# Kernel tuning notes

Measured on AMD Instinct MI355X. Metric: run time of the kernel, lower is better.

The kernel has to match this reference:

```python
import jax, jax.numpy as jnp
import numpy as np

B, S, HID = 1, 4096, 2048
H, KV, D = 16, 4, 128          # query heads, kv heads, head_dim
REP = H // KV                   # GQA group size
SCALE = 0.08838834764831845     # query_pre_attn_scalar (= head_dim**-0.5)
SOFTCAP = 50.0                  # attn_logit_softcapping
NEG = -1e9


def rotate_half(x):
    x1, x2 = jnp.split(x, 2, axis=-1)
    return jnp.concatenate((-x2, x1), axis=-1)


def setup_inputs() -> dict:
    key = jax.random.key(0)
    ks = jax.random.split(key, 8)
    hidden_states = jax.random.normal(ks[0], (B, S, HID), jnp.float32)
    # RoPE tables [B, S, D]
    inv_freq = 1.0 / (10000.0 ** (np.arange(0, D, 2, dtype=np.float32) / D))
    pos = np.arange(S, dtype=np.float32)
    freqs = np.outer(pos, inv_freq)                      # [S, D/2]
    emb = np.concatenate([freqs, freqs], axis=-1)        # [S, D]
    cos = jnp.asarray(np.cos(emb))[None]                 # [1, S, D]
    sin = jnp.asarray(np.sin(emb))[None]
    # additive causal mask [1, 1, S, S]
    causal = jnp.tril(jnp.ones((S, S), jnp.bool_))
    attention_mask = jnp.where(causal, 0.0, NEG)[None, None].astype(jnp.float32)
    wq = jax.random.normal(ks[1], (H * D, HID), jnp.float32) * 0.02
    wk = jax.random.normal(ks[2], (KV * D, HID), jnp.float32) * 0.02
    wv = jax.random.normal(ks[3], (KV * D, HID), jnp.float32) * 0.02
    wo = jax.random.normal(ks[4], (HID, H * D), jnp.float32) * 0.02
    return {"hidden_states": hidden_states, "cos": cos, "sin": sin,
            "attention_mask": attention_mask, "wq": wq, "wk": wk, "wv": wv, "wo": wo}


def reference(hidden_states, cos, sin, attention_mask, wq, wk, wv, wo):
    b, s, _ = hidden_states.shape
    # projections (nn.Linear: x @ W^T)
    q = (hidden_states @ wq.T).reshape(b, s, H, D).transpose(0, 2, 1, 3)   # [b,H,s,D]
    k = (hidden_states @ wk.T).reshape(b, s, KV, D).transpose(0, 2, 1, 3)  # [b,KV,s,D]
    v = (hidden_states @ wv.T).reshape(b, s, KV, D).transpose(0, 2, 1, 3)
    # RoPE (cos/sin broadcast over head dim)
    c = cos[:, None]  # [b,1,s,D]
    sn = sin[:, None]
    q = q * c + rotate_half(q) * sn
    k = k * c + rotate_half(k) * sn
    q = q * SCALE
    # GQA: group query heads instead of materializing repeated K/V
    qg = q.reshape(b, KV, REP, s, D)                                       # [b,g,r,s,D]
    scores = jnp.einsum('bgrqd,bgkd->bgrqk', qg, k)                        # [b,g,r,s,s]
    scores = jnp.tanh(scores / SOFTCAP) * SOFTCAP
    scores = scores + attention_mask[:, :, None]                           # broadcast mask
    probs = jax.nn.softmax(scores.astype(jnp.float32), axis=-1).astype(q.dtype)
    out = jnp.einsum('bgrqk,bgkd->bgrqd', probs, v)                        # [b,g,r,s,D]
    out = out.reshape(b, H, s, D).transpose(0, 2, 1, 3).reshape(b, s, H * D)
    return out @ wo.T
```

## Files before the change

kernel.cpp:

```cpp
#include <hip/hip_runtime.h>
#include <stdint.h>


typedef __attribute__((ext_vector_type(8))) short bf16x8;
typedef __attribute__((ext_vector_type(4))) float f32x4;

#define SCALE_F 0.08838834764831845f

__device__ __forceinline__ ushort f2bf(float f) {
  union { float f; uint32_t u; } v; v.f = f;
  uint32_t r = (v.u + 0x7FFFu + ((v.u >> 16) & 1u)) >> 16;
  return (ushort)r;
}
__device__ __forceinline__ ushort f2bf_fast(float f) {
  union { float f; uint32_t u; } v; v.f = f;
  return (ushort)((v.u + 0x8000u) >> 16);
}
__device__ __forceinline__ float bf2f(ushort u) {
  union { uint32_t u; float f; } v; v.u = ((uint32_t)u) << 16;
  return v.f;
}
__device__ __forceinline__ void gload_lds16(const void* g, void* l) {
  __builtin_amdgcn_global_load_lds((__attribute__((address_space(1))) void*)g,
                                   (__attribute__((address_space(3))) void*)l,
                                   16, 0, 0);
}

__global__ void cvt_kernel(const float* __restrict__ src, ushort* __restrict__ dst, int n4) {
  int idx = blockIdx.x * blockDim.x + threadIdx.x;
  int stride = gridDim.x * blockDim.x;
  for (int i = idx; i < n4; i += stride) {
    float4 v = ((const float4*)src)[i];
    ushort4 o;
    o.x = f2bf(v.x); o.y = f2bf(v.y); o.z = f2bf(v.z); o.w = f2bf(v.w);
    ((ushort4*)dst)[i] = o;
  }
}

template <int MODE>
__global__ __launch_bounds__(256, 2) void gemm_bt(
    const ushort* __restrict__ A, const ushort* __restrict__ B,
    ushort* __restrict__ Cbf, float* __restrict__ Cf, ushort* __restrict__ Vt,
    int M, int N, int K, int ldc) {
  __shared__ ushort As[128 * 64];
  __shared__ ushort Bs[128 * 64];
  const int tid = threadIdx.x;
  const int m0 = blockIdx.y * 128;
  const int n0 = blockIdx.x * 128;
  const int lane = tid & 63, w = tid >> 6;
  const int wr = (w >> 1) * 64, wc = (w & 1) * 64;
  const int fr = lane & 15, fg = lane >> 4;

  const f32x4 vzero = {0.f, 0.f, 0.f, 0.f};
  f32x4 acc[4][4];
#pragma unroll
  for (int i = 0; i < 4; ++i)
#pragma unroll
    for (int j = 0; j < 4; ++j) acc[i][j] = vzero;

  for (int kt = 0; kt < K; kt += 64) {
    __syncthreads();
#pragma unroll
    for (int jj = 0; jj < 4; ++jj) {
      int ci = jj * 256 + tid;
      int r = ci >> 3, c = ci & 7;
      int cs = c ^ (r & 7);
      gload_lds16(A + ((size_t)(m0 + r) * K + kt + cs * 8), &As[ci * 8]);
      gload_lds16(B + ((size_t)(n0 + r) * K + kt + cs * 8), &Bs[ci * 8]);
    }
    __syncthreads();
#pragma unroll
    for (int kk = 0; kk < 2; ++kk) {
      bf16x8 aF[4], bF[4];
#pragma unroll
      for (int i = 0; i < 4; ++i) {
        int r = wr + i * 16 + fr;
        int c = kk * 4 + fg;
        aF[i] = *(const bf16x8*)&As[r * 64 + ((c ^ (r & 7)) * 8)];
      }
#pragma unroll
      for (int j = 0; j < 4; ++j) {
        int r = wc + j * 16 + fr;
        int c = kk * 4 + fg;
        bF[j] = *(const bf16x8*)&Bs[r * 64 + ((c ^ (r & 7)) * 8)];
      }
#pragma unroll
      for (int i = 0; i < 4; ++i)
#pragma unroll
        for (int j = 0; j < 4; ++j)
          acc[i][j] = __builtin_amdgcn_mfma_f32_16x16x32_bf16(aF[i], bF[j], acc[i][j], 0, 0, 0);
    }
  }

  if (MODE == 0) {
    if (n0 < 2560) {
#pragma unroll
      for (int i = 0; i < 4; ++i)
#pragma unroll
        for (int j = 0; j < 4; ++j) {
          int m = m0 + wr + i * 16 + fg * 4;
          int n = n0 + wc + j * 16 + fr;
#pragma unroll
          for (int r = 0; r < 4; ++r)
            Cbf[(size_t)(m + r) * ldc + n] = f2bf(acc[i][j][r]);
        }
    } else {
#pragma unroll
      for (int i = 0; i < 4; ++i)
#pragma unroll
        for (int j = 0; j < 4; ++j) {
          int d = (n0 - 2560) + wc + j * 16 + fr;
          int mB = m0 + wr + i * 16 + fg * 4;
          ushort4 pv;
          pv.x = f2bf(acc[i][j][0]);
          pv.y = f2bf(acc[i][j][1]);
          pv.z = f2bf(acc[i][j][2]);
          pv.w = f2bf(acc[i][j][3]);
          *(ushort4*)&Vt[(size_t)d * 4096 + mB] = pv;
        }
    }
  } else {
#pragma unroll
    for (int i = 0; i < 4; ++i)
#pragma unroll
      for (int j = 0; j < 4; ++j) {
        int m = m0 + wr + i * 16 + fg * 4;
        int n = n0 + wc + j * 16 + fr;
#pragma unroll
        for (int r = 0; r < 4; ++r)
          Cf[(size_t)(m + r) * ldc + n] = acc[i][j][r];
      }
  }
}

__global__ void rope_kernel(ushort* __restrict__ QKV, const float* __restrict__ cosp,
                            const float* __restrict__ sinp) {
  int id = blockIdx.x * blockDim.x + threadIdx.x;
  int s = id / 160;
  int rem = id % 160;
  int head = rem >> 3;
  int d0 = (rem & 7) * 8;
  size_t base = (size_t)s * 2560 + head * 128 + d0;
  bf16x8 lo = *(bf16x8*)&QKV[base];
  bf16x8 hi = *(bf16x8*)&QKV[base + 64];
  const float* cr = cosp + (size_t)s * 128 + d0;
  const float* sr = sinp + (size_t)s * 128 + d0;
  float scale = (head < 16) ? SCALE_F : 1.0f;
  bf16x8 vlo, vhi;
#pragma unroll
  for (int e = 0; e < 8; ++e) {
    float lv = bf2f((ushort)lo[e]);
    float hv = bf2f((ushort)hi[e]);
    float c = cr[e], sn = sr[e];
    float nlo = (lv * c - hv * sn) * scale;
    float nhi = (hv * c + lv * sn) * scale;
    vlo[e] = (short)f2bf(nlo);
    vhi[e] = (short)f2bf(nhi);
  }
  *(bf16x8*)&QKV[base] = vlo;
  *(bf16x8*)&QKV[base + 64] = vhi;
}

__global__ __launch_bounds__(256, 2) void attn_kernel(
    const ushort* __restrict__ QKV, const ushort* __restrict__ Vt,
    ushort* __restrict__ Out) {
  __shared__ ushort Ks[2][64 * 128];
  __shared__ ushort Vs[2][128 * 64];
  __shared__ ushort Ps[4][32 * 64];

  const int tid = threadIdx.x;
  const int x = blockIdx.x;
  const int qb = (x < 256) ? (x >> 4) : (47 - (x >> 4));
  const int h = x & 15;
  const int g = h >> 2;
  const int lane = tid & 63, w = tid >> 6;
  const int fr = lane & 15, fg = lane >> 4;
  const int q0 = qb * 128 + w * 32;

  bf16x8 qf[2][4];
#pragma unroll
  for (int i = 0; i < 2; ++i)
#pragma unroll
    for (int kk = 0; kk < 4; ++kk)
      qf[i][kk] = *(const bf16x8*)&QKV[(size_t)(q0 + i * 16 + fr) * 2560 + h * 128 + kk * 32 + fg * 8];

  const f32x4 vzero = {0.f, 0.f, 0.f, 0.f};
  float lrow[2][4];
  f32x4 Oa[2][8];
#pragma unroll
  for (int i = 0; i < 2; ++i) {
#pragma unroll
    for (int r = 0; r < 4; ++r) lrow[i][r] = 0.f;
#pragma unroll
    for (int jd = 0; jd < 8; ++jd) Oa[i][jd] = vzero;
  }

  const int nt = 2 * qb + 2;
  const size_t kcol = 2048 + (size_t)g * 128;
  const size_t vbase = (size_t)g * 128 * 4096;
  ushort* pw = &Ps[w][0];

  const float K1 = 0.05770780163555854f;
  const float K2 = -144.26950408889634f;

  auto stage = [&](int buf, int t) {
#pragma unroll
    for (int jj = 0; jj < 4; ++jj) {
      int ci = jj * 256 + tid;
      {
        int r = ci >> 4, c = ci & 15;
        int cs = c ^ (r & 7);
        gload_lds16(&QKV[(size_t)(t * 64 + r) * 2560 + kcol + cs * 8], &Ks[buf][ci * 8]);
      }
      {
        int r = ci >> 3, c = ci & 7;
        int cs = c ^ (r & 7);
        gload_lds16(&Vt[vbase + (size_t)r * 4096 + t * 64 + cs * 8], &Vs[buf][ci * 8]);
      }
    }
  };

  stage(0, 0);
  __syncthreads();

  for (int t = 0; t < nt; ++t) {
    const int cur = t & 1;
    if (t + 1 < nt) stage(cur ^ 1, t + 1);

    const bool skipw = (t == nt - 1) && (w < 2);
    if (!skipw) {
      f32x4 sv[2][4];
#pragma unroll
      for (int i = 0; i < 2; ++i)
#pragma unroll
        for (int j = 0; j < 4; ++j) sv[i][j] = vzero;
      __builtin_amdgcn_s_setprio(1);
#pragma unroll
      for (int kk = 0; kk < 4; ++kk) {
#pragma unroll
        for (int j = 0; j < 4; ++j) {
          int r = j * 16 + fr;
          int c = kk * 4 + fg;
          bf16x8 bF = *(const bf16x8*)&Ks[cur][r * 128 + ((c ^ (r & 7)) * 8)];
#pragma unroll
          for (int i = 0; i < 2; ++i)
            sv[i][j] = __builtin_amdgcn_mfma_f32_16x16x32_bf16(qf[i][kk], bF, sv[i][j], 0, 0, 0);
        }
      }
      __builtin_amdgcn_s_setprio(0);

      const bool need_mask = ((t == nt - 2) && (w < 2)) || ((t == nt - 1) && (w >= 2));

#pragma unroll
      for (int i = 0; i < 2; ++i)
#pragma unroll
        for (int j = 0; j < 4; ++j)
#pragma unroll
          for (int r = 0; r < 4; ++r) {
            float v = sv[i][j][r];
            float ex = exp2f(v * K1);
            float p = exp2f(K2 * __builtin_amdgcn_rcpf(ex + 1.0f));
            if (need_mask) {
              int row = q0 + i * 16 + fg * 4 + r;
              int col = t * 64 + j * 16 + fr;
              p = (col > row) ? 0.f : p;
            }
            lrow[i][r] += p;
            sv[i][j][r] = p;
          }

#pragma unroll
      for (int i = 0; i < 2; ++i)
#pragma unroll
        for (int j = 0; j < 4; ++j)
#pragma unroll
          for (int r = 0; r < 4; ++r) {
            int rr = i * 16 + fg * 4 + r;
            int cc = j * 16 + fr;
            int addr = rr * 64 + (((cc >> 3) ^ (rr & 7)) * 8) + (cc & 7);
            pw[addr] = f2bf_fast(sv[i][j][r]);
          }

      __builtin_amdgcn_s_setprio(1);
#pragma unroll
      for (int kk = 0; kk < 2; ++kk) {
        bf16x8 paf[2];
#pragma unroll
        for (int i = 0; i < 2; ++i) {
          int r = i * 16 + fr;
          int c = kk * 4 + fg;
          paf[i] = *(const bf16x8*)&pw[r * 64 + ((c ^ (r & 7)) * 8)];
        }
#pragma unroll
        for (int jd = 0; jd < 8; ++jd) {
          int rv = jd * 16 + fr;
          int c = kk * 4 + fg;
          bf16x8 vF = *(const bf16x8*)&Vs[cur][rv * 64 + ((c ^ (rv & 7)) * 8)];
#pragma unroll
          for (int i = 0; i < 2; ++i)
            Oa[i][jd] = __builtin_amdgcn_mfma_f32_16x16x32_bf16(paf[i], vF, Oa[i][jd], 0, 0, 0);
        }
      }
      __builtin_amdgcn_s_setprio(0);
    }

    __syncthreads();
  }

#pragma unroll
  for (int i = 0; i < 2; ++i)
#pragma unroll
    for (int r = 0; r < 4; ++r) {
      float s = lrow[i][r];
      s += __shfl_xor(s, 1, 64);
      s += __shfl_xor(s, 2, 64);
      s += __shfl_xor(s, 4, 64);
      s += __shfl_xor(s, 8, 64);
      float inv = __builtin_amdgcn_rcpf(s);
      int m = q0 + i * 16 + fg * 4 + r;
#pragma unroll
      for (int jd = 0; jd < 8; ++jd)
        Out[(size_t)m * 2048 + h * 128 + jd * 16 + fr] = f2bf(Oa[i][jd][r] * inv);
    }
}

extern "C" void kernel_launch(void* const* d_in, const int* in_sizes, int n_in,
                              void* d_out, int out_size, void* d_ws, size_t ws_size,
                              hipStream_t stream) {
  const float* hidden = (const float*)d_in[0];
  const float* cosp = (const float*)d_in[1];
  const float* sinp = (const float*)d_in[2];
  const float* wq = (const float*)d_in[4];
  const float* wk = (const float*)d_in[5];
  const float* wv = (const float*)d_in[6];
  const float* wo = (const float*)d_in[7];
  float* out = (float*)d_out;

  char* ws = (char*)d_ws;
  ushort* Xb = (ushort*)(ws);
  ushort* Wqkv = (ushort*)(ws + 16777216);
  ushort* Wob = (ushort*)(ws + 16777216 + 12582912);
  ushort* QKV = (ushort*)(ws + 16777216 + 12582912 + 8388608);
  ushort* Vtb = (ushort*)(ws + 16777216 + 12582912 + 8388608 + 20971520);
  ushort* AttnO = Xb;

  cvt_kernel<<<2048, 256, 0, stream>>>(hidden, Xb, (4096 * 2048) / 4);
  cvt_kernel<<<1024, 256, 0, stream>>>(wq, Wqkv, (2048 * 2048) / 4);
  cvt_kernel<<<512, 256, 0, stream>>>(wk, Wqkv + 2048 * 2048, (512 * 2048) / 4);
  cvt_kernel<<<512, 256, 0, stream>>>(wv, Wqkv + 2560 * 2048, (512 * 2048) / 4);
  cvt_kernel<<<1024, 256, 0, stream>>>(wo, Wob, (2048 * 2048) / 4);

  gemm_bt<0><<<dim3(24, 32), 256, 0, stream>>>(Xb, Wqkv, QKV, nullptr, Vtb,
                                               4096, 3072, 2048, 2560);
  rope_kernel<<<2560, 256, 0, stream>>>(QKV, cosp, sinp);
  attn_kernel<<<512, 256, 0, stream>>>(QKV, Vtb, AttnO);
  gemm_bt<1><<<dim3(16, 32), 256, 0, stream>>>(AttnO, Wob, nullptr, out, nullptr,
                                               4096, 2048, 2048, 2048);
}
```

Measured before the change: 437.3 us.

## Split causal attention KV range across two blocks and add normalization pass

Each (query block, head) pair now launches as two blocks, each covering half of the causal key tiles. Each half writes unnormalized fp32 partial outputs and row sums to workspace, and a new norm_kernel adds the halves, divides by the row sums and converts to bf16. Because the softcapped softmax uses a fixed maximum, the partial sums can be added directly without rescaling. The aim is more blocks and better load balance across CUs, at the cost of extra fp32 memory traffic and an additional kernel launch. The split path runs only when the workspace is large enough to hold the partial buffers.

```diff
diff --git a/kernel.cpp b/kernel.cpp
--- a/kernel.cpp
+++ b/kernel.cpp
@@ -161,17 +161,26 @@
   *(bf16x8*)&QKV[base + 64] = vhi;
 }
 
+template <int SPLIT>
 __global__ __launch_bounds__(256, 2) void attn_kernel(
     const ushort* __restrict__ QKV, const ushort* __restrict__ Vt,
-    ushort* __restrict__ Out) {
+    ushort* __restrict__ Out, float* __restrict__ pO, float* __restrict__ pl) {
   __shared__ ushort Ks[2][64 * 128];
   __shared__ ushort Vs[2][128 * 64];
   __shared__ ushort Ps[4][32 * 64];
 
   const int tid = threadIdx.x;
   const int x = blockIdx.x;
-  const int qb = (x < 256) ? (x >> 4) : (47 - (x >> 4));
-  const int h = x & 15;
+  int qb, h, c;
+  if (SPLIT) {
+    qb = 31 - (x >> 5);
+    h = x & 15;
+    c = (x >> 4) & 1;
+  } else {
+    qb = (x < 256) ? (x >> 4) : (47 - (x >> 4));
+    h = x & 15;
+    c = 0;
+  }
   const int g = h >> 2;
   const int lane = tid & 63, w = tid >> 6;
   const int fr = lane & 15, fg = lane >> 4;
@@ -196,6 +205,8 @@
   }
 
   const int nt = 2 * qb + 2;
+  const int t0 = SPLIT ? c * (qb + 1) : 0;
+  const int t1 = SPLIT ? (t0 + qb + 1) : nt;
   const size_t kcol = 2048 + (size_t)g * 128;
   const size_t vbase = (size_t)g * 128 * 4096;
   ushort* pw = &Ps[w][0];
@@ -208,24 +219,24 @@
     for (int jj = 0; jj < 4; ++jj) {
       int ci = jj * 256 + tid;
       {
-        int r = ci >> 4, c = ci & 15;
-        int cs = c ^ (r & 7);
+        int r = ci >> 4, cc = ci & 15;
+        int cs = cc ^ (r & 7);
         gload_lds16(&QKV[(size_t)(t * 64 + r) * 2560 + kcol + cs * 8], &Ks[buf][ci * 8]);
       }
       {
-        int r = ci >> 3, c = ci & 7;
-        int cs = c ^ (r & 7);
+        int r = ci >> 3, cc = ci & 7;
+        int cs = cc ^ (r & 7);
         gload_lds16(&Vt[vbase + (size_t)r * 4096 + t * 64 + cs * 8], &Vs[buf][ci * 8]);
       }
     }
   };
 
-  stage(0, 0);
+  stage(0, t0);
   __syncthreads();
 
-  for (int t = 0; t < nt; ++t) {
-    const int cur = t & 1;
-    if (t + 1 < nt) stage(cur ^ 1, t + 1);
+  for (int t = t0; t < t1; ++t) {
+    const int cur = (t - t0) & 1;
+    if (t + 1 < t1) stage(cur ^ 1, t + 1);
 
     const bool skipw = (t == nt - 1) && (w < 2);
     if (!skipw) {
@@ -240,8 +251,8 @@
 #pragma unroll
         for (int j = 0; j < 4; ++j) {
           int r = j * 16 + fr;
-          int c = kk * 4 + fg;
-          bf16x8 bF = *(const bf16x8*)&Ks[cur][r * 128 + ((c ^ (r & 7)) * 8)];
+          int cc = kk * 4 + fg;
+          bf16x8 bF = *(const bf16x8*)&Ks[cur][r * 128 + ((cc ^ (r & 7)) * 8)];
 #pragma unroll
           for (int i = 0; i < 2; ++i)
             sv[i][j] = __builtin_amdgcn_mfma_f32_16x16x32_bf16(qf[i][kk], bF, sv[i][j], 0, 0, 0);
@@ -288,14 +299,14 @@
 #pragma unroll
         for (int i = 0; i < 2; ++i) {
           int r = i * 16 + fr;
-          int c = kk * 4 + fg;
-          paf[i] = *(const bf16x8*)&pw[r * 64 + ((c ^ (r & 7)) * 8)];
+          int cc = kk * 4 + fg;
+          paf[i] = *(const bf16x8*)&pw[r * 64 + ((cc ^ (r & 7)) * 8)];
         }
 #pragma unroll
         for (int jd = 0; jd < 8; ++jd) {
           int rv = jd * 16 + fr;
-          int c = kk * 4 + fg;
-          bf16x8 vF = *(const bf16x8*)&Vs[cur][rv * 64 + ((c ^ (rv & 7)) * 8)];
+          int cc = kk * 4 + fg;
+          bf16x8 vF = *(const bf16x8*)&Vs[cur][rv * 64 + ((cc ^ (rv & 7)) * 8)];
 #pragma unroll
           for (int i = 0; i < 2; ++i)
             Oa[i][jd] = __builtin_amdgcn_mfma_f32_16x16x32_bf16(paf[i], vF, Oa[i][jd], 0, 0, 0);
@@ -307,21 +318,58 @@
     __syncthreads();
   }
 
-#pragma unroll
-  for (int i = 0; i < 2; ++i)
-#pragma unroll
-    for (int r = 0; r < 4; ++r) {
-      float s = lrow[i][r];
-      s += __shfl_xor(s, 1, 64);
-      s += __shfl_xor(s, 2, 64);
-      s += __shfl_xor(s, 4, 64);
-      s += __shfl_xor(s, 8, 64);
-      float inv = __builtin_amdgcn_rcpf(s);
-      int m = q0 + i * 16 + fg * 4 + r;
-#pragma unroll
-      for (int jd = 0; jd < 8; ++jd)
-        Out[(size_t)m * 2048 + h * 128 + jd * 16 + fr] = f2bf(Oa[i][jd][r] * inv);
-    }
+  if (SPLIT) {
+    float* pOc = pO + (size_t)c * 4096 * 2048;
+#pragma unroll
+    for (int i = 0; i < 2; ++i)
+#pragma unroll
+      for (int r = 0; r < 4; ++r) {
+        float s = lrow[i][r];
+        s += __shfl_xor(s, 1, 64);
+        s += __shfl_xor(s, 2, 64);
+        s += __shfl_xor(s, 4, 64);
+        s += __shfl_xor(s, 8, 64);
+        int m = q0 + i * 16 + fg * 4 + r;
+        if (fr == 0) pl[(size_t)c * 4096 * 16 + m * 16 + h] = s;
+#pragma unroll
+        for (int jd = 0; jd < 8; ++jd)
+          pOc[(size_t)m * 2048 + h * 128 + jd * 16 + fr] = Oa[i][jd][r];
+      }
+  } else {
+#pragma unroll
+    for (int i = 0; i < 2; ++i)
+#pragma unroll
+      for (int r = 0; r < 4; ++r) {
+        float s = lrow[i][r];
+        s += __shfl_xor(s, 1, 64);
+        s += __shfl_xor(s, 2, 64);
+        s += __shfl_xor(s, 4, 64);
+        s += __shfl_xor(s, 8, 64);
+        float inv = __builtin_amdgcn_rcpf(s);
+        int m = q0 + i * 16 + fg * 4 + r;
+#pragma unroll
+        for (int jd = 0; jd < 8; ++jd)
+          Out[(size_t)m * 2048 + h * 128 + jd * 16 + fr] = f2bf(Oa[i][jd][r] * inv);
+      }
+  }
+}
+
+__global__ void norm_kernel(const float* __restrict__ pO, const float* __restrict__ pl,
+                            ushort* __restrict__ Out) {
+  int i = blockIdx.x * blockDim.x + threadIdx.x;
+  int col = (i * 4) & 2047;
+  int m = (i * 4) >> 11;
+  int h = col >> 7;
+  float l = pl[m * 16 + h] + pl[4096 * 16 + m * 16 + h];
+  float inv = __builtin_amdgcn_rcpf(l);
+  float4 a = ((const float4*)pO)[i];
+  float4 b = ((const float4*)pO)[i + (4096 * 2048 / 4)];
+  ushort4 o;
+  o.x = f2bf((a.x + b.x) * inv);
+  o.y = f2bf((a.y + b.y) * inv);
+  o.z = f2bf((a.z + b.z) * inv);
+  o.w = f2bf((a.w + b.w) * inv);
+  ((ushort4*)Out)[i] = o;
 }
 
 extern "C" void kernel_launch(void* const* d_in, const int* in_sizes, int n_in,
@@ -337,11 +385,15 @@
   float* out = (float*)d_out;
 
   char* ws = (char*)d_ws;
-  ushort* Xb = (ushort*)(ws);
-  ushort* Wqkv = (ushort*)(ws + 16777216);
-  ushort* Wob = (ushort*)(ws + 16777216 + 12582912);
-  ushort* QKV = (ushort*)(ws + 16777216 + 12582912 + 8388608);
-  ushort* Vtb = (ushort*)(ws + 16777216 + 12582912 + 8388608 + 20971520);
+  size_t off = 0;
+  ushort* Xb = (ushort*)(ws + off); off += (size_t)4096 * 2048 * 2;
+  ushort* Wqkv = (ushort*)(ws + off); off += (size_t)3072 * 2048 * 2;
+  ushort* Wob = (ushort*)(ws + off); off += (size_t)2048 * 2048 * 2;
+  ushort* QKV = (ushort*)(ws + off); off += (size_t)4096 * 2560 * 2;
+  ushort* Vtb = (ushort*)(ws + off); off += (size_t)512 * 4096 * 2;
+  float* pO = (float*)(ws + off); off += (size_t)2 * 4096 * 2048 * 4;
+  float* pl = (float*)(ws + off); off += (size_t)2 * 4096 * 16 * 4;
+  const bool use_split = (ws_size >= off);
   ushort* AttnO = Xb;
 
   cvt_kernel<<<2048, 256, 0, stream>>>(hidden, Xb, (4096 * 2048) / 4);
@@ -353,7 +405,12 @@
   gemm_bt<0><<<dim3(24, 32), 256, 0, stream>>>(Xb, Wqkv, QKV, nullptr, Vtb,
                                                4096, 3072, 2048, 2560);
   rope_kernel<<<2560, 256, 0, stream>>>(QKV, cosp, sinp);
-  attn_kernel<<<512, 256, 0, stream>>>(QKV, Vtb, AttnO);
+  if (use_split) {
+    attn_kernel<1><<<1024, 256, 0, stream>>>(QKV, Vtb, nullptr, pO, pl);
+    norm_kernel<<<(4096 * 2048 / 4) / 256, 256, 0, stream>>>(pO, pl, AttnO);
+  } else {
+    attn_kernel<0><<<512, 256, 0, stream>>>(QKV, Vtb, AttnO, nullptr, nullptr);
+  }
   gemm_bt<1><<<dim3(16, 32), 256, 0, stream>>>(AttnO, Wob, nullptr, out, nullptr,
                                                4096, 2048, 2048, 2048);
 }
```

Measured after the change: 411.1 us. 6.0% less time.
